# Kernel optimization log

Measured on AMD Instinct MI355X. Metric: run time of the kernel, lower is better.

Reference implementation:

```python
import jax, jax.numpy as jnp
import numpy as np

N = 8192          # number of nodes
E = 524288        # number of edges (avg degree 64)
D = 256           # latent_dim
NEG_FILL = -1e9   # torch.full fill value


def setup_inputs() -> dict:
    key = jax.random.key(0)
    k1, k2, k3, k4, k5, k6 = jax.random.split(key, 6)
    encoded = jax.random.normal(k1, (N, D), dtype=jnp.float32)
    h = jax.random.normal(k2, (N, D), dtype=jnp.float32)
    edge_index = jax.random.randint(k3, (2, E), 0, N, dtype=jnp.int64)
    edge_attr = jax.random.normal(k4, (E,), dtype=jnp.float32)
    # Linear weights (bias=False); stored as [in, out] for x @ W
    W1 = jax.random.normal(k5, (2 * D + 1, D), dtype=jnp.float32) * (1.0 / np.sqrt(2 * D + 1))
    W2 = jax.random.normal(k6, (D, 1), dtype=jnp.float32) * (1.0 / np.sqrt(D))
    return {"encoded": encoded, "h": h, "edge_index": edge_index,
            "edge_attr": edge_attr, "W1": W1, "W2": W2}


def reference(encoded, h, edge_index, edge_attr, W1, W2):
    left, right = edge_index[0], edge_index[1]
    # gather endpoint states and concat with scalar edge feature -> [E, 2D+1]
    feats = jnp.concatenate([h[left], h[right], edge_attr[:, None]], axis=1)
    # 2-layer MLP (no bias): Linear -> ReLU -> Linear -> [E]
    scores = (jax.nn.relu(feats @ W1) @ W2)[:, 0]
    # scatter into dense (N, N) matrix prefilled with -1e9
    result = jnp.full((h.shape[0], h.shape[0]), NEG_FILL, dtype=h.dtype)
    return result.at[left, right].set(scores)
```

## Files before the change

### kernel.cpp

```cpp
#include <hip/hip_runtime.h>

#define N_NODES 8192
#define E_EDGES 524288
#define D_DIM   256
#define NEG_FILL -1e9f

#define PROJ_BLOCKS 256
#define ROWS_PER_BLOCK 32
#define FILL_BLOCKS 1792

#define EDGE_BLOCKS 2048
#define EDGES_PER_WAVE 64

typedef float vfloat4 __attribute__((ext_vector_type(4)));
typedef float vfloat2 __attribute__((ext_vector_type(2)));

__global__ __launch_bounds__(256) void fill_proj_kernel(
    const float* __restrict__ h,
    const float* __restrict__ W1,
    float* __restrict__ out,
    unsigned char* __restrict__ AB)
{
    if (blockIdx.x < PROJ_BLOCKS) {
        const int t  = threadIdx.x;
        const int r0 = blockIdx.x * ROWS_PER_BLOCK;

        float accA[ROWS_PER_BLOCK];
        float accB[ROWS_PER_BLOCK];
        #pragma unroll
        for (int r = 0; r < ROWS_PER_BLOCK; ++r) { accA[r] = 0.f; accB[r] = 0.f; }

        for (int k = 0; k < D_DIM; k += 4) {
            float wa0 = W1[(k + 0) * D_DIM + t];
            float wa1 = W1[(k + 1) * D_DIM + t];
            float wa2 = W1[(k + 2) * D_DIM + t];
            float wa3 = W1[(k + 3) * D_DIM + t];
            float wb0 = W1[(256 + k + 0) * D_DIM + t];
            float wb1 = W1[(256 + k + 1) * D_DIM + t];
            float wb2 = W1[(256 + k + 2) * D_DIM + t];
            float wb3 = W1[(256 + k + 3) * D_DIM + t];
            #pragma unroll
            for (int r = 0; r < ROWS_PER_BLOCK; ++r) {
                const float4 hv = *(const float4*)&h[(r0 + r) * D_DIM + k];
                accA[r] = fmaf(hv.x, wa0, accA[r]);
                accA[r] = fmaf(hv.y, wa1, accA[r]);
                accA[r] = fmaf(hv.z, wa2, accA[r]);
                accA[r] = fmaf(hv.w, wa3, accA[r]);
                accB[r] = fmaf(hv.x, wb0, accB[r]);
                accB[r] = fmaf(hv.y, wb1, accB[r]);
                accB[r] = fmaf(hv.z, wb2, accB[r]);
                accB[r] = fmaf(hv.w, wb3, accB[r]);
            }
        }

        unsigned char* A = AB;
        unsigned char* B = AB + (long long)N_NODES * D_DIM;
        #pragma unroll
        for (int r = 0; r < ROWS_PER_BLOCK; ++r) {
            int pa = __builtin_amdgcn_cvt_pk_fp8_f32(accA[r], accA[r], 0, false);
            int pb = __builtin_amdgcn_cvt_pk_fp8_f32(accB[r], accB[r], 0, false);
            A[(long long)(r0 + r) * D_DIM + t] = (unsigned char)(pa & 0xFF);
            B[(long long)(r0 + r) * D_DIM + t] = (unsigned char)(pb & 0xFF);
        }
    } else {
        const int b = blockIdx.x - PROJ_BLOCKS;
        const int nvec = (N_NODES / 4) * N_NODES;
        vfloat4 fv = { NEG_FILL, NEG_FILL, NEG_FILL, NEG_FILL };
        vfloat4* o4 = (vfloat4*)out;
        for (int i = b * 256 + threadIdx.x; i < nvec; i += FILL_BLOCKS * 256)
            __builtin_nontemporal_store(fv, &o4[i]);
    }
}

__global__ __launch_bounds__(256) void edge_kernel(
    const int* __restrict__ eidx,
    const float* __restrict__ eattr,
    const float* __restrict__ W1,
    const float* __restrict__ W2,
    const unsigned char* __restrict__ AB,
    float* __restrict__ out)
{
    const int wave = blockIdx.x * 4 + (threadIdx.x >> 6);
    const int lane = threadIdx.x & 63;
    const int g    = lane >> 4;
    const int t    = lane & 15;
    const int base = wave * EDGES_PER_WAVE;

    const int   l_all = __builtin_nontemporal_load(&eidx[base + lane]);
    const int   r_all = __builtin_nontemporal_load(&eidx[E_EDGES + base + lane]);
    const float a_all = __builtin_nontemporal_load(&eattr[base + lane]);
    const int   lr_all = (l_all << 13) | r_all;

    const int j0 = t * 16;
    vfloat2 wl[8], w2[8];
    const vfloat2* wlp = (const vfloat2*)&W1[512 * D_DIM + j0];
    const vfloat2* w2p = (const vfloat2*)&W2[j0];
    #pragma unroll
    for (int i = 0; i < 8; ++i) { wl[i] = wlp[i]; w2[i] = w2p[i]; }
    const unsigned char* Bt = AB + (long long)N_NODES * D_DIM;
    const vfloat2 zero2 = { 0.f, 0.f };

    int   lr_c = __shfl(lr_all, g);
    float at_c = __shfl(a_all, g);
    uint4 av_c = *(const uint4*)(AB + (unsigned)(lr_c >> 13) * D_DIM + j0);
    uint4 bv_c = *(const uint4*)(Bt + (unsigned)(lr_c & 8191) * D_DIM + j0);

    #pragma unroll 4
    for (int i = 0; i < EDGES_PER_WAVE / 4; ++i) {
        const int   lr_cur = lr_c;
        const float attr   = at_c;
        const uint4 av     = av_c;
        const uint4 bv     = bv_c;
        if (i + 1 < EDGES_PER_WAVE / 4) {
            lr_c = __shfl(lr_all, 4 * (i + 1) + g);
            at_c = __shfl(a_all, 4 * (i + 1) + g);
            av_c = *(const uint4*)(AB + (unsigned)(lr_c >> 13) * D_DIM + j0);
            bv_c = *(const uint4*)(Bt + (unsigned)(lr_c & 8191) * D_DIM + j0);
        }

        const vfloat2 attr2 = { attr, attr };
        vfloat2 s2 = zero2;
        #define MLP_STEP(AV, BV, WL01, WL23, W201, W223) {                         \
            vfloat2 alo = __builtin_amdgcn_cvt_pk_f32_fp8((int)(AV), false);       \
            vfloat2 ahi = __builtin_amdgcn_cvt_pk_f32_fp8((int)(AV), true);        \
            vfloat2 blo = __builtin_amdgcn_cvt_pk_f32_fp8((int)(BV), false);       \
            vfloat2 bhi = __builtin_amdgcn_cvt_pk_f32_fp8((int)(BV), true);        \
            vfloat2 h01 = __builtin_elementwise_fma(attr2, WL01, alo + blo);       \
            h01 = __builtin_elementwise_max(h01, zero2);                           \
            s2  = __builtin_elementwise_fma(h01, W201, s2);                        \
            vfloat2 h23 = __builtin_elementwise_fma(attr2, WL23, ahi + bhi);       \
            h23 = __builtin_elementwise_max(h23, zero2);                           \
            s2  = __builtin_elementwise_fma(h23, W223, s2);                        \
        }
        MLP_STEP(av.x, bv.x, wl[0], wl[1], w2[0], w2[1]);
        MLP_STEP(av.y, bv.y, wl[2], wl[3], w2[2], w2[3]);
        MLP_STEP(av.z, bv.z, wl[4], wl[5], w2[4], w2[5]);
        MLP_STEP(av.w, bv.w, wl[6], wl[7], w2[6], w2[7]);
        #undef MLP_STEP

        float s = s2.x + s2.y;
        s += __shfl_xor(s, 8);
        s += __shfl_xor(s, 4);
        s += __shfl_xor(s, 2);
        s += __shfl_xor(s, 1);

        if (t == 0)
            __builtin_nontemporal_store(s, &out[(unsigned)lr_cur]);
    }
}

extern "C" void kernel_launch(void* const* d_in, const int* in_sizes, int n_in,
                              void* d_out, int out_size, void* d_ws, size_t ws_size,
                              hipStream_t stream) {
    const float* h     = (const float*)d_in[1];
    const int*   eidx  = (const int*)d_in[2];
    const float* eattr = (const float*)d_in[3];
    const float* W1    = (const float*)d_in[4];
    const float* W2    = (const float*)d_in[5];
    float* out = (float*)d_out;
    unsigned char* AB = (unsigned char*)d_ws;

    fill_proj_kernel<<<PROJ_BLOCKS + FILL_BLOCKS, 256, 0, stream>>>(h, W1, out, AB);
    edge_kernel<<<EDGE_BLOCKS, 256, 0, stream>>>(eidx, eattr, W1, W2, AB, out);
}
```

Before: 431.8 us.

## Compute node projections with bf16 MFMA and interleave projection blocks with fill blocks

The per-node projections h@W1a and h@W1b were computed with scalar FP32 FMAs. They now use bf16 16x16x32 MFMA instructions, 512 projection blocks of 16 rows each. Projection blocks are interleaved with fill blocks (every fourth block), so the matrix work overlaps the bandwidth-bound -1e9 fill instead of running as a front-loaded group. This drops projection precision to bf16 before the fp8 quantization, uses uncoalesced strided loads of W1 per MFMA tile, and leaves fewer fill blocks (1536).

```diff
diff --git a/kernel.cpp b/kernel.cpp
--- a/kernel.cpp
+++ b/kernel.cpp
@@ -5,15 +5,15 @@
 #define D_DIM   256
 #define NEG_FILL -1e9f
 
-#define PROJ_BLOCKS 256
-#define ROWS_PER_BLOCK 32
-#define FILL_BLOCKS 1792
+#define K1_BLOCKS 2048
 
 #define EDGE_BLOCKS 2048
 #define EDGES_PER_WAVE 64
 
-typedef float vfloat4 __attribute__((ext_vector_type(4)));
-typedef float vfloat2 __attribute__((ext_vector_type(2)));
+typedef float  vfloat4 __attribute__((ext_vector_type(4)));
+typedef float  vfloat2 __attribute__((ext_vector_type(2)));
+typedef float  f32x4   __attribute__((ext_vector_type(4)));
+typedef __bf16 bf16x8  __attribute__((ext_vector_type(8)));
 
 __global__ __launch_bounds__(256) void fill_proj_kernel(
     const float* __restrict__ h,
@@ -21,53 +21,63 @@
     float* __restrict__ out,
     unsigned char* __restrict__ AB)
 {
-    if (blockIdx.x < PROJ_BLOCKS) {
-        const int t  = threadIdx.x;
-        const int r0 = blockIdx.x * ROWS_PER_BLOCK;
+    if ((blockIdx.x & 3) == 3) {
+        const int r0   = (blockIdx.x >> 2) * 16;
+        const int w    = threadIdx.x >> 6;
+        const int lane = threadIdx.x & 63;
+        const int lrow = lane & 15;
+        const int kgrp = lane >> 4;
+        const int col0 = w * 128;
 
-        float accA[ROWS_PER_BLOCK];
-        float accB[ROWS_PER_BLOCK];
+        f32x4 acc[8];
         #pragma unroll
-        for (int r = 0; r < ROWS_PER_BLOCK; ++r) { accA[r] = 0.f; accB[r] = 0.f; }
+        for (int nt = 0; nt < 8; ++nt) acc[nt] = (f32x4){0.f, 0.f, 0.f, 0.f};
 
-        for (int k = 0; k < D_DIM; k += 4) {
-            float wa0 = W1[(k + 0) * D_DIM + t];
-            float wa1 = W1[(k + 1) * D_DIM + t];
-            float wa2 = W1[(k + 2) * D_DIM + t];
-            float wa3 = W1[(k + 3) * D_DIM + t];
-            float wb0 = W1[(256 + k + 0) * D_DIM + t];
-            float wb1 = W1[(256 + k + 1) * D_DIM + t];
-            float wb2 = W1[(256 + k + 2) * D_DIM + t];
-            float wb3 = W1[(256 + k + 3) * D_DIM + t];
+        for (int ks = 0; ks < 8; ++ks) {
+            const int k0 = ks * 32 + kgrp * 8;
+
+            const float* ap = &h[(r0 + lrow) * D_DIM + k0];
+            const float4 a0 = *(const float4*)ap;
+            const float4 a1 = *(const float4*)(ap + 4);
+            bf16x8 af;
+            af[0] = (__bf16)a0.x; af[1] = (__bf16)a0.y;
+            af[2] = (__bf16)a0.z; af[3] = (__bf16)a0.w;
+            af[4] = (__bf16)a1.x; af[5] = (__bf16)a1.y;
+            af[6] = (__bf16)a1.z; af[7] = (__bf16)a1.w;
+
             #pragma unroll
-            for (int r = 0; r < ROWS_PER_BLOCK; ++r) {
-                const float4 hv = *(const float4*)&h[(r0 + r) * D_DIM + k];
-                accA[r] = fmaf(hv.x, wa0, accA[r]);
-                accA[r] = fmaf(hv.y, wa1, accA[r]);
-                accA[r] = fmaf(hv.z, wa2, accA[r]);
-                accA[r] = fmaf(hv.w, wa3, accA[r]);
-                accB[r] = fmaf(hv.x, wb0, accB[r]);
-                accB[r] = fmaf(hv.y, wb1, accB[r]);
-                accB[r] = fmaf(hv.z, wb2, accB[r]);
-                accB[r] = fmaf(hv.w, wb3, accB[r]);
+            for (int nt = 0; nt < 8; ++nt) {
+                const int c = col0 + nt * 16 + lrow;
+                const float* bp = (c < 256)
+                    ? &W1[(long long)k0 * D_DIM + c]
+                    : &W1[(long long)(256 + k0) * D_DIM + (c - 256)];
+                bf16x8 bf;
+                #pragma unroll
+                for (int i = 0; i < 8; ++i) bf[i] = (__bf16)bp[i * D_DIM];
+                acc[nt] = __builtin_amdgcn_mfma_f32_16x16x32_bf16(af, bf, acc[nt], 0, 0, 0);
             }
         }
 
         unsigned char* A = AB;
         unsigned char* B = AB + (long long)N_NODES * D_DIM;
         #pragma unroll
-        for (int r = 0; r < ROWS_PER_BLOCK; ++r) {
-            int pa = __builtin_amdgcn_cvt_pk_fp8_f32(accA[r], accA[r], 0, false);
-            int pb = __builtin_amdgcn_cvt_pk_fp8_f32(accB[r], accB[r], 0, false);
-            A[(long long)(r0 + r) * D_DIM + t] = (unsigned char)(pa & 0xFF);
-            B[(long long)(r0 + r) * D_DIM + t] = (unsigned char)(pb & 0xFF);
+        for (int nt = 0; nt < 8; ++nt) {
+            const int c = col0 + nt * 16 + lrow;
+            #pragma unroll
+            for (int q = 0; q < 4; ++q) {
+                const int row = r0 + kgrp * 4 + q;
+                const float v = acc[nt][q];
+                int p = __builtin_amdgcn_cvt_pk_fp8_f32(v, v, 0, false);
+                if (c < 256) A[(long long)row * D_DIM + c]         = (unsigned char)(p & 0xFF);
+                else         B[(long long)row * D_DIM + (c - 256)] = (unsigned char)(p & 0xFF);
+            }
         }
     } else {
-        const int b = blockIdx.x - PROJ_BLOCKS;
+        const int b = (blockIdx.x >> 2) * 3 + (blockIdx.x & 3);
         const int nvec = (N_NODES / 4) * N_NODES;
         vfloat4 fv = { NEG_FILL, NEG_FILL, NEG_FILL, NEG_FILL };
         vfloat4* o4 = (vfloat4*)out;
-        for (int i = b * 256 + threadIdx.x; i < nvec; i += FILL_BLOCKS * 256)
+        for (int i = b * 256 + threadIdx.x; i < nvec; i += 1536 * 256)
             __builtin_nontemporal_store(fv, &o4[i]);
     }
 }
@@ -160,6 +170,6 @@
     float* out = (float*)d_out;
     unsigned char* AB = (unsigned char*)d_ws;
 
-    fill_proj_kernel<<<PROJ_BLOCKS + FILL_BLOCKS, 256, 0, stream>>>(h, W1, out, AB);
+    fill_proj_kernel<<<K1_BLOCKS, 256, 0, stream>>>(h, W1, out, AB);
     edge_kernel<<<EDGE_BLOCKS, 256, 0, stream>>>(eidx, eattr, W1, W2, AB, out);
 }
```

Result: faster. 369.5 us (-14.4%).
